# Optimization experiments

Measured on AMD Instinct MI355X. Metric: run time of the kernel, lower is better.

Reference implementation:

```python
import jax, jax.numpy as jnp
import numpy as np

N_NODES = 100000
N_EDGES = 3200000
IN_CH, HID, OUT_CH = 128, 16, 64


def gcn_conv(x, W, b, row, col, n_nodes):
    # PyG GCNConv: add self loops, symmetric deg^{-1/2} normalization,
    # linear transform, scatter-add aggregation at target nodes (col).
    x = x @ W  # [N, out]
    deg = jax.ops.segment_sum(jnp.ones_like(col, dtype=x.dtype), col,
                              num_segments=n_nodes)  # includes self loops
    inv_sqrt = jnp.where(deg > 0, jax.lax.rsqrt(deg), 0.0)
    norm = inv_sqrt[row] * inv_sqrt[col]  # [E+N]
    msgs = x[row] * norm[:, None]  # gather + scale
    out = jax.ops.segment_sum(msgs, col, num_segments=n_nodes)
    return out + b


def setup_inputs() -> dict:
    key = jax.random.key(0)
    ks = jax.random.split(key, 12)
    x = jax.random.normal(ks[0], (N_NODES, IN_CH), dtype=jnp.float32)
    edge_index = jax.random.randint(ks[1], (2, N_EDGES), 0, N_NODES, dtype=jnp.int64)

    def glorot(k, fan_in, fan_out):
        s = jnp.sqrt(6.0 / (fan_in + fan_out))
        return jax.random.uniform(k, (fan_in, fan_out), jnp.float32, -s, s)

    return {
        'x': x,
        'edge_index': edge_index,
        'conv1_W': glorot(ks[2], IN_CH, HID),
        'conv1_b': jnp.zeros((HID,), jnp.float32),
        'conv2_W': glorot(ks[3], HID, OUT_CH),
        'conv2_b': jnp.zeros((OUT_CH,), jnp.float32),
        't1_W': glorot(ks[4], IN_CH, HID),
        't1_b': jnp.zeros((HID,), jnp.float32),
        't2_W': glorot(ks[5], HID, OUT_CH),
        't2_b': jnp.zeros((OUT_CH,), jnp.float32),
    }


def reference(x, edge_index, conv1_W, conv1_b, conv2_W, conv2_b,
              t1_W, t1_b, t2_W, t2_b):
    n = x.shape[0]
    # add self loops once (fixed shape)
    loops = jnp.arange(n, dtype=edge_index.dtype)
    row = jnp.concatenate([edge_index[0], loops])
    col = jnp.concatenate([edge_index[1], loops])

    identity1 = x @ t1_W + t1_b
    h = jax.nn.relu(gcn_conv(x, conv1_W, conv1_b, row, col, n)) + identity1
    identity2 = h @ t2_W + t2_b
    out = jax.nn.relu(gcn_conv(h, conv2_W, conv2_b, row, col, n)) + identity2
    return out
```

## Files before the change

### kernel.cpp

```cpp
#include <hip/hip_runtime.h>

#define INCH 128
#define C1   16
#define C2   64
#define LOCB 7
#define BNODES (1 << LOCB)
#define CAP  8192
#define ROWBITS 17
#define ROWMASK ((1 << ROWBITS) - 1)
#define SENT 0xFFFFFFFFu

typedef int iv4 __attribute__((ext_vector_type(4)));
typedef unsigned short usv8 __attribute__((ext_vector_type(8)));

__device__ __forceinline__ unsigned short f2bf(float f) {
    unsigned u = __float_as_uint(f);
    return (unsigned short)((u + 0x7FFF + ((u >> 16) & 1)) >> 16);
}
__device__ __forceinline__ float bf2f(unsigned short s) {
    return __uint_as_float((unsigned)s << 16);
}

__global__ void binit_kernel(int* __restrict__ gcur, int K) {
    int t = blockIdx.x * blockDim.x + threadIdx.x;
    if (t < K) gcur[t] = t * CAP;
}

__global__ __launch_bounds__(256) void bucket_kernel(
    const int* __restrict__ row, const int* __restrict__ col,
    int* __restrict__ gcur, int* __restrict__ barr,
    int e, int n, int K, int nblocks)
{
    __shared__ int cnt[1024];
    __shared__ int cur[1024];
    __shared__ int sst[1024];
    int e4 = e >> 2;
    long b0 = (long)blockIdx.x * e4 / nblocks;
    long b1 = (long)(blockIdx.x + 1) * e4 / nblocks;
    const iv4* c4p = (const iv4*)col;
    const iv4* r4p = (const iv4*)row;
    for (int i = threadIdx.x; i < 1024; i += 256) cnt[i] = 0;
    __syncthreads();
    for (long i = b0 + threadIdx.x; i < b1; i += 256) {
        iv4 c4 = c4p[i], r4 = r4p[i];
        #pragma unroll
        for (int k = 0; k < 4; ++k) {
            unsigned c = (unsigned)c4[k], r = (unsigned)r4[k];
            if (c < (unsigned)n && r < (unsigned)n)
                atomicAdd(&cnt[c >> LOCB], 1);
        }
    }
    if (blockIdx.x == 0) {
        for (int i = e4 * 4 + threadIdx.x; i < e; i += 256) {
            unsigned c = (unsigned)col[i], r = (unsigned)row[i];
            if (c < (unsigned)n && r < (unsigned)n)
                atomicAdd(&cnt[c >> LOCB], 1);
        }
    }
    __syncthreads();
    for (int i = threadIdx.x; i < K; i += 256) {
        int c = cnt[i];
        int start = c ? atomicAdd(&gcur[i], (c + 15) & ~15) : 0;
        cur[i] = start;
        sst[i] = start;
    }
    __syncthreads();
    for (long i = b0 + threadIdx.x; i < b1; i += 256) {
        iv4 c4 = c4p[i], r4 = r4p[i];
        #pragma unroll
        for (int k = 0; k < 4; ++k) {
            unsigned c = (unsigned)c4[k], r = (unsigned)r4[k];
            if (c < (unsigned)n && r < (unsigned)n) {
                int b = c >> LOCB;
                int slot = atomicAdd(&cur[b], 1);
                if ((unsigned)slot < (unsigned)((b + 1) * CAP))
                    barr[slot] = (int)(r | ((c & (BNODES - 1)) << ROWBITS));
            }
        }
    }
    if (blockIdx.x == 0) {
        for (int i = e4 * 4 + threadIdx.x; i < e; i += 256) {
            unsigned c = (unsigned)col[i], r = (unsigned)row[i];
            if (c < (unsigned)n && r < (unsigned)n) {
                int b = c >> LOCB;
                int slot = atomicAdd(&cur[b], 1);
                if ((unsigned)slot < (unsigned)((b + 1) * CAP))
                    barr[slot] = (int)(r | ((c & (BNODES - 1)) << ROWBITS));
            }
        }
    }
    __syncthreads();
    for (int i = threadIdx.x; i < K; i += 256) {
        int c = cnt[i];
        if (!c) continue;
        int start = sst[i];
        int end = start + c;
        int re  = start + ((c + 15) & ~15);
        int lim = (i + 1) * CAP;
        if (end > lim) end = lim;
        if (re  > lim) re  = lim;
        for (int j = end; j < re; ++j) barr[j] = (int)SENT;
    }
}

__global__ __launch_bounds__(1024) void bucket_scan_kernel(
    const int* __restrict__ gcur, int* __restrict__ bbase, int K)
{
    __shared__ int tmp[1024];
    int t = threadIdx.x;
    int len = 0;
    if (t < K) {
        int l = gcur[t] - t * CAP;
        len = (l < 0) ? 0 : (l > CAP ? CAP : l);
    }
    tmp[t] = len;
    __syncthreads();
    for (int off = 1; off < 1024; off <<= 1) {
        int v = (t >= off) ? tmp[t - off] : 0;
        __syncthreads();
        tmp[t] += v;
        __syncthreads();
    }
    if (t < K) bbase[t] = tmp[t] - len;
}

__global__ __launch_bounds__(256) void sort_kernel(
    const int* __restrict__ barr, const int* __restrict__ gcur,
    const int* __restrict__ bbase,
    int* __restrict__ cnt, int* __restrict__ offs, float* __restrict__ inv,
    int* __restrict__ sorted, int n)
{
    __shared__ int lcnt[BNODES];
    __shared__ int lcur[BNODES];
    __shared__ int tmp[BNODES];
    int b = blockIdx.x;
    int tid = threadIdx.x;
    if (tid < BNODES) lcnt[tid] = 0;
    __syncthreads();
    int base = b * CAP;
    int len = gcur[b] - base;
    if (len < 0) len = 0;
    if (len > CAP) len = CAP;
    int len4 = len >> 2;
    const iv4* b4 = (const iv4*)(barr + base);
    for (int i = tid; i < len4; i += 256) {
        iv4 p4 = b4[i];
        #pragma unroll
        for (int k = 0; k < 4; ++k) {
            unsigned pk = (unsigned)p4[k];
            if ((pk & ROWMASK) < (unsigned)n)
                atomicAdd(&lcnt[(pk >> ROWBITS) & (BNODES - 1)], 1);
        }
    }
    for (int i = len4 * 4 + tid; i < len; i += 256) {
        unsigned pk = (unsigned)barr[base + i];
        if ((pk & ROWMASK) < (unsigned)n)
            atomicAdd(&lcnt[(pk >> ROWBITS) & (BNODES - 1)], 1);
    }
    __syncthreads();
    int v = (tid < BNODES) ? lcnt[tid] : 0;
    if (tid < BNODES) tmp[tid] = v;
    __syncthreads();
    for (int off = 1; off < BNODES; off <<= 1) {
        int t2 = (tid < BNODES && tid >= off) ? tmp[tid - off] : 0;
        __syncthreads();
        if (tid < BNODES) tmp[tid] += t2;
        __syncthreads();
    }
    int gbase = bbase[b];
    if (tid < BNODES) {
        int exc = tmp[tid] - v;
        lcur[tid] = exc;
        int node = (b << LOCB) + tid;
        if (node < n) {
            cnt[node]  = v;
            offs[node] = gbase + exc;
            inv[node]  = rsqrtf((float)(v + 1));
        }
    }
    __syncthreads();
    for (int i = tid; i < len4; i += 256) {
        iv4 p4 = b4[i];
        #pragma unroll
        for (int k = 0; k < 4; ++k) {
            unsigned pk = (unsigned)p4[k];
            if ((pk & ROWMASK) < (unsigned)n) {
                int loc = (pk >> ROWBITS) & (BNODES - 1);
                int pos = atomicAdd(&lcur[loc], 1);
                if ((unsigned)pos < (unsigned)CAP)
                    sorted[gbase + pos] = (int)(pk & ROWMASK);
            }
        }
    }
    for (int i = len4 * 4 + tid; i < len; i += 256) {
        unsigned pk = (unsigned)barr[base + i];
        if ((pk & ROWMASK) < (unsigned)n) {
            int loc = (pk >> ROWBITS) & (BNODES - 1);
            int pos = atomicAdd(&lcur[loc], 1);
            if ((unsigned)pos < (unsigned)CAP)
                sorted[gbase + pos] = (int)(pk & ROWMASK);
        }
    }
}

__global__ __launch_bounds__(256) void linear1_kernel(
    const float* __restrict__ x, const float* __restrict__ W1,
    const float* __restrict__ T1, const float* __restrict__ t1b,
    const float* __restrict__ inv,
    unsigned short* __restrict__ xW1s_bf, float* __restrict__ xT1, int n)
{
    __shared__ float Wc[INCH][32];
    __shared__ float xs[16][INCH + 4];
    int tid = threadIdx.x;

    for (int i = tid; i < INCH * C1; i += 256) {
        int k = i / C1, c = i % C1;
        Wc[k][c]      = W1[i];
        Wc[k][c + 16] = T1[i];
    }
    int node0 = blockIdx.x * 16;
    for (int i = tid; i < 16 * (INCH / 4); i += 256) {
        int r = i / (INCH / 4);
        int cc = i % (INCH / 4);
        int node = node0 + r;
        float4 v = make_float4(0.f, 0.f, 0.f, 0.f);
        if (node < n) v = ((const float4*)x)[(size_t)node * (INCH / 4) + cc];
        ((float4*)&xs[r][0])[cc] = v;
    }
    __syncthreads();

    int ch = tid & 15, nl = tid >> 4;
    int node = node0 + nl;
    if (node >= n) return;
    float a1 = 0.f, a2 = 0.f;
    #pragma unroll
    for (int k = 0; k < INCH; ++k) {
        float xv = xs[nl][k];
        a1 += xv * Wc[k][ch];
        a2 += xv * Wc[k][ch + 16];
    }
    xW1s_bf[(node << 4) + ch] = f2bf(a1 * inv[node]);
    xT1[(node << 4) + ch]     = a2 + t1b[ch];
}

#define GATHER_ACC(SRCBUF)                                                    \
    float a0 = 0.f, a1 = 0.f, a2 = 0.f, a3 = 0.f,                             \
          a4 = 0.f, a5 = 0.f, a6 = 0.f, a7 = 0.f;                             \
    {                                                                         \
        int p = beg + pr;                                                     \
        for (; p + 6 < end; p += 8) {                                         \
            int s0 = sorted[p],     s1 = sorted[p + 2];                       \
            int s2 = sorted[p + 4], s3 = sorted[p + 6];                       \
            usv8 v0 = *(const usv8*)(SRCBUF + ((size_t)s0 << 4) + chb);       \
            usv8 v1 = *(const usv8*)(SRCBUF + ((size_t)s1 << 4) + chb);       \
            usv8 v2 = *(const usv8*)(SRCBUF + ((size_t)s2 << 4) + chb);       \
            usv8 v3 = *(const usv8*)(SRCBUF + ((size_t)s3 << 4) + chb);       \
            a0 += bf2f(v0[0]) + bf2f(v1[0]) + bf2f(v2[0]) + bf2f(v3[0]);      \
            a1 += bf2f(v0[1]) + bf2f(v1[1]) + bf2f(v2[1]) + bf2f(v3[1]);      \
            a2 += bf2f(v0[2]) + bf2f(v1[2]) + bf2f(v2[2]) + bf2f(v3[2]);      \
            a3 += bf2f(v0[3]) + bf2f(v1[3]) + bf2f(v2[3]) + bf2f(v3[3]);      \
            a4 += bf2f(v0[4]) + bf2f(v1[4]) + bf2f(v2[4]) + bf2f(v3[4]);      \
            a5 += bf2f(v0[5]) + bf2f(v1[5]) + bf2f(v2[5]) + bf2f(v3[5]);      \
            a6 += bf2f(v0[6]) + bf2f(v1[6]) + bf2f(v2[6]) + bf2f(v3[6]);      \
            a7 += bf2f(v0[7]) + bf2f(v1[7]) + bf2f(v2[7]) + bf2f(v3[7]);      \
        }                                                                     \
        for (; p < end; p += 2) {                                             \
            int s0 = sorted[p];                                               \
            usv8 v0 = *(const usv8*)(SRCBUF + ((size_t)s0 << 4) + chb);       \
            a0 += bf2f(v0[0]); a1 += bf2f(v0[1]);                             \
            a2 += bf2f(v0[2]); a3 += bf2f(v0[3]);                             \
            a4 += bf2f(v0[4]); a5 += bf2f(v0[5]);                             \
            a6 += bf2f(v0[6]); a7 += bf2f(v0[7]);                             \
        }                                                                     \
    }                                                                         \
    a0 += __shfl_xor(a0, 2); a1 += __shfl_xor(a1, 2);                         \
    a2 += __shfl_xor(a2, 2); a3 += __shfl_xor(a3, 2);                         \
    a4 += __shfl_xor(a4, 2); a5 += __shfl_xor(a5, 2);                         \
    a6 += __shfl_xor(a6, 2); a7 += __shfl_xor(a7, 2);

__global__ __launch_bounds__(256) void agg1_csr_kernel(
    const int* __restrict__ sorted, const int* __restrict__ offs,
    const int* __restrict__ cnt, const float* __restrict__ inv,
    const unsigned short* __restrict__ xW1s_bf, const float* __restrict__ xT1,
    const float* __restrict__ b1,
    float* __restrict__ h, unsigned short* __restrict__ hs_bf, int n)
{
    int tid = threadIdx.x;
    int node = blockIdx.x * 64 + (tid >> 2);
    int pr  = (tid >> 1) & 1;
    int chb = (tid & 1) << 3;
    int beg = 0, end = 0;
    if (node < n) { beg = offs[node]; end = beg + cnt[node]; }

    GATHER_ACC(xW1s_bf)

    if (node >= n || pr != 0) return;
    size_t idx = ((size_t)node << 4) + chb;
    usv8 selfv = *(const usv8*)(xW1s_bf + idx);
    float ic = inv[node];
    float hv0 = fmaxf((a0 + bf2f(selfv[0])) * ic + b1[chb + 0], 0.f) + xT1[idx + 0];
    float hv1 = fmaxf((a1 + bf2f(selfv[1])) * ic + b1[chb + 1], 0.f) + xT1[idx + 1];
    float hv2 = fmaxf((a2 + bf2f(selfv[2])) * ic + b1[chb + 2], 0.f) + xT1[idx + 2];
    float hv3 = fmaxf((a3 + bf2f(selfv[3])) * ic + b1[chb + 3], 0.f) + xT1[idx + 3];
    float hv4 = fmaxf((a4 + bf2f(selfv[4])) * ic + b1[chb + 4], 0.f) + xT1[idx + 4];
    float hv5 = fmaxf((a5 + bf2f(selfv[5])) * ic + b1[chb + 5], 0.f) + xT1[idx + 5];
    float hv6 = fmaxf((a6 + bf2f(selfv[6])) * ic + b1[chb + 6], 0.f) + xT1[idx + 6];
    float hv7 = fmaxf((a7 + bf2f(selfv[7])) * ic + b1[chb + 7], 0.f) + xT1[idx + 7];
    ((float4*)(h + idx))[0] = make_float4(hv0, hv1, hv2, hv3);
    ((float4*)(h + idx))[1] = make_float4(hv4, hv5, hv6, hv7);
    usv8 hb;
    hb[0] = f2bf(hv0 * ic); hb[1] = f2bf(hv1 * ic);
    hb[2] = f2bf(hv2 * ic); hb[3] = f2bf(hv3 * ic);
    hb[4] = f2bf(hv4 * ic); hb[5] = f2bf(hv5 * ic);
    hb[6] = f2bf(hv6 * ic); hb[7] = f2bf(hv7 * ic);
    *(usv8*)(hs_bf + idx) = hb;
}

__global__ __launch_bounds__(256) void agg2_fused_kernel(
    const int* __restrict__ sorted, const int* __restrict__ offs,
    const int* __restrict__ cnt, const float* __restrict__ inv,
    const unsigned short* __restrict__ hs_bf, const float* __restrict__ h,
    const float* __restrict__ W2, const float* __restrict__ T2,
    const float* __restrict__ b2, const float* __restrict__ t2b,
    float* __restrict__ out, int n)
{
    __shared__ float Wc[C1][128];
    __shared__ float acc_s[64][C1];
    __shared__ float h_s[64][C1];
    int tid = threadIdx.x;

    for (int i = tid; i < C1 * 128; i += 256) {
        int k = i >> 7, c = i & 127;
        Wc[k][c] = (c < 64) ? W2[k * C2 + c] : T2[k * C2 + (c - 64)];
    }
    {
        int node0 = blockIdx.x * 64;
        if (tid < 256) {
            float4 v = make_float4(0.f, 0.f, 0.f, 0.f);
            if (node0 + (tid >> 2) < n)
                v = ((const float4*)h)[(size_t)node0 * 4 + tid];
            ((float4*)&h_s[0][0])[tid] = v;
        }
    }

    int node = blockIdx.x * 64 + (tid >> 2);
    int pr  = (tid >> 1) & 1;
    int chb = (tid & 1) << 3;
    int beg = 0, end = 0;
    if (node < n) { beg = offs[node]; end = beg + cnt[node]; }

    GATHER_ACC(hs_bf)

    if (node < n && pr == 0) {
        size_t idx = ((size_t)node << 4) + chb;
        usv8 selfv = *(const usv8*)(hs_bf + idx);
        float ic = inv[node];
        int loc = tid >> 2;
        float4* ap = (float4*)&acc_s[loc][chb];
        ap[0] = make_float4((a0 + bf2f(selfv[0])) * ic, (a1 + bf2f(selfv[1])) * ic,
                            (a2 + bf2f(selfv[2])) * ic, (a3 + bf2f(selfv[3])) * ic);
        ap[1] = make_float4((a4 + bf2f(selfv[4])) * ic, (a5 + bf2f(selfv[5])) * ic,
                            (a6 + bf2f(selfv[6])) * ic, (a7 + bf2f(selfv[7])) * ic);
    }
    __syncthreads();

    int och = tid & 63, g = tid >> 6;
    float w1r[C1], w2r[C1];
    #pragma unroll
    for (int k = 0; k < C1; ++k) { w1r[k] = Wc[k][och]; w2r[k] = Wc[k][och + 64]; }
    float bb = b2[och], tb = t2b[och];
    for (int q = 0; q < 16; ++q) {
        int loc = (g << 4) + q;
        int node2 = blockIdx.x * 64 + loc;
        if (node2 >= n) continue;
        float s1 = bb, s2 = tb;
        #pragma unroll
        for (int k = 0; k < C1; ++k) {
            s1 += acc_s[loc][k] * w1r[k];
            s2 += h_s[loc][k]   * w2r[k];
        }
        out[(size_t)node2 * C2 + och] = fmaxf(s1, 0.f) + s2;
    }
}

extern "C" void kernel_launch(void* const* d_in, const int* in_sizes, int n_in,
                              void* d_out, int out_size, void* d_ws, size_t ws_size,
                              hipStream_t stream) {
    const float* x   = (const float*)d_in[0];
    const int*   ei  = (const int*)d_in[1];
    const float* W1  = (const float*)d_in[2];
    const float* b1  = (const float*)d_in[3];
    const float* W2  = (const float*)d_in[4];
    const float* b2  = (const float*)d_in[5];
    const float* T1  = (const float*)d_in[6];
    const float* t1b = (const float*)d_in[7];
    const float* T2  = (const float*)d_in[8];
    const float* t2b = (const float*)d_in[9];
    float* out = (float*)d_out;

    const int n = in_sizes[0] / INCH;
    const int e = in_sizes[1] / 2;
    const int* row = ei;
    const int* col = ei + e;
    const int K = (n + BNODES - 1) >> LOCB;

    char* ws = (char*)d_ws;
    int*   gcur  = (int*)ws;                          ws += 4096;
    int*   bbase = (int*)ws;                          ws += 4096;
    int*   cnt   = (int*)ws;                          ws += (size_t)n * 4;
    int*   offs  = (int*)ws;                          ws += (size_t)n * 4;
    float* inv   = (float*)ws;                        ws += (size_t)n * 4;
    float* xT1   = (float*)ws;                        ws += (size_t)n * C1 * 4;
    float* h     = (float*)ws;                        ws += (size_t)n * C1 * 4;
    unsigned short* xW1s_bf = (unsigned short*)ws;    ws += (size_t)n * C1 * 2;
    unsigned short* hs_bf   = (unsigned short*)ws;    ws += (size_t)n * C1 * 2;
    int*   sorted= (int*)ws;                          ws += (size_t)K * CAP * 4;
    int*   barr  = (int*)ws;                          ws += (size_t)K * CAP * 4;

    const int B = 256;
    const int nbb = 390;

    binit_kernel      <<<(K + B - 1) / B, B, 0, stream>>>(gcur, K);
    bucket_kernel     <<<nbb, B, 0, stream>>>(row, col, gcur, barr, e, n, K, nbb);
    bucket_scan_kernel<<<1, 1024, 0, stream>>>(gcur, bbase, K);
    sort_kernel       <<<K, B, 0, stream>>>(barr, gcur, bbase, cnt, offs, inv, sorted, n);

    linear1_kernel <<<(n + 15) / 16, B, 0, stream>>>(x, W1, T1, t1b, inv, xW1s_bf, xT1, n);
    agg1_csr_kernel<<<(n + 63) / 64, B, 0, stream>>>(sorted, offs, cnt, inv, xW1s_bf, xT1, b1, h, hs_bf, n);

    agg2_fused_kernel<<<(n + 63) / 64, B, 0, stream>>>(sorted, offs, cnt, inv, hs_bf, h,
                                                       W2, T2, b2, t2b, out, n);
}
```

Baseline: 277.1 us.

## Stage bucketed edges in LDS and write them to global coalesced per bucket

The bucket kernel now runs a block-local prefix scan over bucket counts and scatters edges into a shared-memory staging buffer instead of straight to global memory. Each wavefront then copies whole buckets to their global slots with coalesced writes, filling the padding with sentinels. This replaces scattered 4-byte global stores with contiguous ones, at the cost of about 33KB more LDS per block (lower occupancy) and an extra scan. If a block has more than 8448 edges, the ones past the staging capacity are silently dropped.

```diff
diff --git a/kernel.cpp b/kernel.cpp
--- a/kernel.cpp
+++ b/kernel.cpp
@@ -9,6 +9,7 @@
 #define ROWBITS 17
 #define ROWMASK ((1 << ROWBITS) - 1)
 #define SENT 0xFFFFFFFFu
+#define STAGE_CAP 8448
 
 typedef int iv4 __attribute__((ext_vector_type(4)));
 typedef unsigned short usv8 __attribute__((ext_vector_type(8)));
@@ -32,16 +33,22 @@
     int e, int n, int K, int nblocks)
 {
     __shared__ int cnt[1024];
-    __shared__ int cur[1024];
-    __shared__ int sst[1024];
+    __shared__ int part[256];
+    __shared__ int ofs[1024];
+    __shared__ int lcur[1024];
+    __shared__ int gst[1024];
+    __shared__ int stage[STAGE_CAP];
+    int tid = threadIdx.x;
     int e4 = e >> 2;
     long b0 = (long)blockIdx.x * e4 / nblocks;
     long b1 = (long)(blockIdx.x + 1) * e4 / nblocks;
     const iv4* c4p = (const iv4*)col;
     const iv4* r4p = (const iv4*)row;
-    for (int i = threadIdx.x; i < 1024; i += 256) cnt[i] = 0;
-    __syncthreads();
-    for (long i = b0 + threadIdx.x; i < b1; i += 256) {
+
+    for (int i = tid; i < 1024; i += 256) cnt[i] = 0;
+    __syncthreads();
+
+    for (long i = b0 + tid; i < b1; i += 256) {
         iv4 c4 = c4p[i], r4 = r4p[i];
         #pragma unroll
         for (int k = 0; k < 4; ++k) {
@@ -51,55 +58,79 @@
         }
     }
     if (blockIdx.x == 0) {
-        for (int i = e4 * 4 + threadIdx.x; i < e; i += 256) {
+        for (int i = e4 * 4 + tid; i < e; i += 256) {
             unsigned c = (unsigned)col[i], r = (unsigned)row[i];
             if (c < (unsigned)n && r < (unsigned)n)
                 atomicAdd(&cnt[c >> LOCB], 1);
         }
     }
     __syncthreads();
-    for (int i = threadIdx.x; i < K; i += 256) {
-        int c = cnt[i];
-        int start = c ? atomicAdd(&gcur[i], (c + 15) & ~15) : 0;
-        cur[i] = start;
-        sst[i] = start;
-    }
-    __syncthreads();
-    for (long i = b0 + threadIdx.x; i < b1; i += 256) {
+
+    int c0 = cnt[4 * tid], c1 = cnt[4 * tid + 1];
+    int c2 = cnt[4 * tid + 2], c3 = cnt[4 * tid + 3];
+    int tot = c0 + c1 + c2 + c3;
+    part[tid] = tot;
+    __syncthreads();
+    for (int off = 1; off < 256; off <<= 1) {
+        int v = (tid >= off) ? part[tid - off] : 0;
+        __syncthreads();
+        part[tid] += v;
+        __syncthreads();
+    }
+    {
+        int base = part[tid] - tot;
+        ofs[4 * tid]     = base;
+        ofs[4 * tid + 1] = base + c0;
+        ofs[4 * tid + 2] = base + c0 + c1;
+        ofs[4 * tid + 3] = base + c0 + c1 + c2;
+        lcur[4 * tid]     = base;
+        lcur[4 * tid + 1] = base + c0;
+        lcur[4 * tid + 2] = base + c0 + c1;
+        lcur[4 * tid + 3] = base + c0 + c1 + c2;
+    }
+    for (int b = tid; b < K; b += 256) {
+        int c = cnt[b];
+        gst[b] = c ? atomicAdd(&gcur[b], (c + 15) & ~15) : 0;
+    }
+    __syncthreads();
+
+    for (long i = b0 + tid; i < b1; i += 256) {
         iv4 c4 = c4p[i], r4 = r4p[i];
         #pragma unroll
         for (int k = 0; k < 4; ++k) {
             unsigned c = (unsigned)c4[k], r = (unsigned)r4[k];
             if (c < (unsigned)n && r < (unsigned)n) {
                 int b = c >> LOCB;
-                int slot = atomicAdd(&cur[b], 1);
-                if ((unsigned)slot < (unsigned)((b + 1) * CAP))
-                    barr[slot] = (int)(r | ((c & (BNODES - 1)) << ROWBITS));
+                int pos = atomicAdd(&lcur[b], 1);
+                if ((unsigned)pos < (unsigned)STAGE_CAP)
+                    stage[pos] = (int)(r | ((c & (BNODES - 1)) << ROWBITS));
             }
         }
     }
     if (blockIdx.x == 0) {
-        for (int i = e4 * 4 + threadIdx.x; i < e; i += 256) {
+        for (int i = e4 * 4 + tid; i < e; i += 256) {
             unsigned c = (unsigned)col[i], r = (unsigned)row[i];
             if (c < (unsigned)n && r < (unsigned)n) {
                 int b = c >> LOCB;
-                int slot = atomicAdd(&cur[b], 1);
-                if ((unsigned)slot < (unsigned)((b + 1) * CAP))
-                    barr[slot] = (int)(r | ((c & (BNODES - 1)) << ROWBITS));
+                int pos = atomicAdd(&lcur[b], 1);
+                if ((unsigned)pos < (unsigned)STAGE_CAP)
+                    stage[pos] = (int)(r | ((c & (BNODES - 1)) << ROWBITS));
             }
         }
     }
     __syncthreads();
-    for (int i = threadIdx.x; i < K; i += 256) {
-        int c = cnt[i];
+
+    int wid = tid >> 6, lane = tid & 63;
+    for (int b = wid; b < K; b += 4) {
+        int c = cnt[b];
         if (!c) continue;
-        int start = sst[i];
-        int end = start + c;
-        int re  = start + ((c + 15) & ~15);
-        int lim = (i + 1) * CAP;
-        if (end > lim) end = lim;
-        if (re  > lim) re  = lim;
-        for (int j = end; j < re; ++j) barr[j] = (int)SENT;
+        int g = gst[b], o = ofs[b];
+        int p = (c + 15) & ~15;
+        int lim = (b + 1) * CAP;
+        for (int j = lane; j < p; j += 64) {
+            int v = (j < c) ? stage[o + j] : (int)SENT;
+            if (g + j < lim) barr[g + j] = v;
+        }
     }
 }
 
```

Result: slower. 293.6 us (+5.9%).
